# Performance work log

Measured on AMD Instinct MI355X. Metric: run time of the kernel, lower is better.

The kernel has to match this reference:

```python
import jax, jax.numpy as jnp
import numpy as np

N, E = 4096, 32768
NI, EI, D, EH = 64, 16, 64, 128
NUM_STEPS = 3


def setup_inputs() -> dict:
    key = jax.random.key(0)
    ks = jax.random.split(key, 24)

    def w(k, shape, fan_in):
        return (jax.random.normal(k, shape, jnp.float32) / np.float32(np.sqrt(fan_in)))

    return {
        "node_feats": jax.random.normal(ks[0], (N, NI), jnp.float32),
        "edge_attr": jax.random.normal(ks[1], (E, EI), jnp.float32),
        "edge_index": jax.random.randint(ks[2], (2, E), 0, N),
        # project_node_feats: Linear(NI -> D)
        "W_p": w(ks[3], (NI, D), NI), "b_p": jnp.zeros((D,), jnp.float32),
        # project_edge_feats: Linear(EI -> EH)
        "W_pe": w(ks[4], (EI, EH), EI), "b_pe": jnp.zeros((EH,), jnp.float32),
        # edge_network (NNConv nn): Linear(EH -> D*D)
        "W_nn": w(ks[5], (EH, D * D), EH), "b_nn": jnp.zeros((D * D,), jnp.float32),
        # NNConv root weight + bias
        "W_root": w(ks[6], (D, D), D), "b_conv": jnp.zeros((D,), jnp.float32),
        # GRU (single layer), gate order r, z, n as in torch
        "w_ih": w(ks[7], (D, 3 * D), D), "w_hh": w(ks[8], (D, 3 * D), D),
        "b_ih": jnp.zeros((3 * D,), jnp.float32), "b_hh": jnp.zeros((3 * D,), jnp.float32),
        # edge_update_network: Linear(EH+2D -> EH), Linear(EH -> EH)
        "W_eu1": w(ks[9], (EH + 2 * D, EH), EH + 2 * D), "b_eu1": jnp.zeros((EH,), jnp.float32),
        "W_eu2": w(ks[10], (EH, EH), EH), "b_eu2": jnp.zeros((EH,), jnp.float32),
    }


def reference(node_feats, edge_attr, edge_index, W_p, b_p, W_pe, b_pe,
              W_nn, b_nn, W_root, b_conv, w_ih, w_hh, b_ih, b_hh,
              W_eu1, b_eu1, W_eu2, b_eu2):
    relu = jax.nn.relu
    row, col = edge_index[0], edge_index[1]  # source, target
    n_nodes = node_feats.shape[0]
    d = W_root.shape[0]

    h = relu(node_feats @ W_p + b_p)          # (N, D) projected node feats
    hidden = h                                  # GRU hidden state
    e = relu(edge_attr @ W_pe + b_pe)          # (E, EH) projected edge feats

    for _ in range(NUM_STEPS):
        # NNConv: per-edge weight matrix from edge MLP (dropout=0 in eval)
        We = relu(e @ W_nn + b_nn).reshape(-1, d, d)      # (E, D, D)
        msg = jnp.einsum('ed,edf->ef', h[row], We)        # gather + per-edge matmul
        agg = jax.ops.segment_sum(msg, col, num_segments=n_nodes)  # scatter-add
        m = relu(agg + h @ W_root + b_conv)                # conv output + activation

        # GRU cell (torch gate order: r, z, n)
        gi = m @ w_ih + b_ih
        gh = hidden @ w_hh + b_hh
        ir, iz, i_n = jnp.split(gi, 3, axis=-1)
        hr, hz, h_n = jnp.split(gh, 3, axis=-1)
        r = jax.nn.sigmoid(ir + hr)
        z = jax.nn.sigmoid(iz + hz)
        ncand = jnp.tanh(i_n + r * h_n)
        hidden = (1.0 - z) * ncand + z * hidden
        h = hidden

        # edge update: cat(h[row], h[col], e) -> 2-layer MLP
        ei = jnp.concatenate([h[row], h[col], e], axis=1)
        e = relu(relu(ei @ W_eu1 + b_eu1) @ W_eu2 + b_eu2)

    return h, e
```

## Files before the change

### kernel.cpp

```cpp
#include <hip/hip_runtime.h>
#include <stdint.h>

typedef __attribute__((ext_vector_type(8))) _Float16 f16x8;
typedef __attribute__((ext_vector_type(4))) float f32x4;

#define N_NODES 4096
#define N_EDGES 32768

__device__ __forceinline__ float sigm(float x) { return 1.f / (1.f + __expf(-x)); }

__device__ __forceinline__ f16x8 packh8(const float* p) {
  f16x8 r;
#pragma unroll
  for (int i = 0; i < 8; ++i) r[i] = (_Float16)p[i];
  return r;
}

__global__ void prep_all(const float* __restrict__ Wnn,
                         const float* __restrict__ We1,
                         const float* __restrict__ We2,
                         _Float16* __restrict__ WnnT,
                         _Float16* __restrict__ We1T,
                         _Float16* __restrict__ We2T) {
  __shared__ float tile[128][33];
  const int b = blockIdx.x, t = threadIdx.x;
  if (b < 128) {
    const int nb = b * 32;
    for (int i = 0; i < 16; ++i) {
      int g = i * 256 + t;
      int k = g >> 5, j = g & 31;
      tile[k][j] = Wnn[(size_t)k * 4096 + nb + j];
    }
    __syncthreads();
    for (int i = 0; i < 16; ++i) {
      int g = i * 256 + t;
      int j = g >> 7, k = g & 127;
      WnnT[(size_t)(nb + j) * 128 + k] = (_Float16)tile[k][j];
    }
  } else {
    int idx = (b - 128) * 256 + t;
    if (idx < 32768) {
      int n = idx >> 8, k = idx & 255;
      We1T[idx] = (_Float16)We1[(size_t)k * 128 + n];
    } else {
      int j = idx - 32768;
      int n = j >> 7, k = j & 127;
      We2T[j] = (_Float16)We2[(size_t)k * 128 + n];
    }
  }
}

__global__ void csr_zero(int* __restrict__ rowcnt) {
  rowcnt[blockIdx.x * 256 + threadIdx.x] = 0;
}
__global__ void csr_count(const int* __restrict__ eidx, int* __restrict__ rowcnt) {
  int e = blockIdx.x * 256 + threadIdx.x;
  atomicAdd(&rowcnt[eidx[N_EDGES + e]], 1);
}
__global__ void csr_scan(const int* __restrict__ rowcnt,
                         int* __restrict__ rowptr, int* __restrict__ cursor) {
  __shared__ int part[1024];
  const int t = threadIdx.x;
  const int base = t * 4;
  int s0 = rowcnt[base], s1 = rowcnt[base + 1], s2 = rowcnt[base + 2], s3 = rowcnt[base + 3];
  int sum = s0 + s1 + s2 + s3;
  part[t] = sum;
  __syncthreads();
  for (int off = 1; off < 1024; off <<= 1) {
    int v = (t >= off) ? part[t - off] : 0;
    __syncthreads();
    part[t] += v;
    __syncthreads();
  }
  int excl = part[t] - sum;
  int p0 = excl, p1 = excl + s0, p2 = excl + s0 + s1, p3 = excl + s0 + s1 + s2;
  rowptr[base] = p0; rowptr[base + 1] = p1; rowptr[base + 2] = p2; rowptr[base + 3] = p3;
  cursor[base] = p0; cursor[base + 1] = p1; cursor[base + 2] = p2; cursor[base + 3] = p3;
  if (t == 0) rowptr[4096] = N_EDGES;
}
__global__ void csr_fill(const int* __restrict__ eidx, int* __restrict__ cursor,
                         int* __restrict__ eids) {
  int e = blockIdx.x * 256 + threadIdx.x;
  int slot = atomicAdd(&cursor[eidx[N_EDGES + e]], 1);
  eids[slot] = e;
}

__global__ void proj_node_f(const float* __restrict__ nf,
                            const float* __restrict__ Wp,
                            const float* __restrict__ bp,
                            float* __restrict__ h) {
  int idx = blockIdx.x * 256 + threadIdx.x;
  int n = idx >> 6, c = idx & 63;
  float acc = bp[c];
  for (int k = 0; k < 64; ++k)
    acc = fmaf(nf[n * 64 + k], Wp[k * 64 + c], acc);
  h[idx] = fmaxf(acc, 0.f);
}

__launch_bounds__(256)
__global__ void proj_edge_f2(const float* __restrict__ ea,
                             const float* __restrict__ Wpe,
                             const float* __restrict__ bpe,
                             float* __restrict__ e) {
  __shared__ float sw[16 * 128];
  __shared__ float sb[128];
  __shared__ float sa[32][17];
  const int t = threadIdx.x;
  const int ebase = blockIdx.x * 32;
  for (int g = t; g < 2048; g += 256) sw[g] = Wpe[g];
  if (t < 128) sb[t] = bpe[t];
  for (int g = t; g < 512; g += 256) {
    int r = g >> 4, k = g & 15;
    sa[r][k] = ea[(size_t)(ebase + r) * 16 + k];
  }
  __syncthreads();
  int c = t & 127, eg = t >> 7;
  float wc[16];
#pragma unroll
  for (int k = 0; k < 16; ++k) wc[k] = sw[k * 128 + c];
  float bv = sb[c];
#pragma unroll
  for (int i = 0; i < 16; ++i) {
    int ee = eg * 16 + i;
    float acc = bv;
#pragma unroll
    for (int k = 0; k < 16; ++k) acc = fmaf(sa[ee][k], wc[k], acc);
    e[(size_t)(ebase + ee) * 128 + c] = fmaxf(acc, 0.f);
  }
}

__launch_bounds__(512, 1)
__global__ void fused_msg_m(const float* __restrict__ ebf,
                            const float* __restrict__ hid,
                            const _Float16* __restrict__ WnnT,
                            const float* __restrict__ bnn,
                            const int* __restrict__ eidx,
                            _Float16* __restrict__ msgbuf) {
  __shared__ __align__(16) _Float16 Ae[128 * 128];
  __shared__ __align__(16) float Hs[64 * 132];
  const int t = threadIdx.x;
  const int w = t >> 6, l = t & 63, l15 = l & 15, q = l >> 4;
  const int fw = w & 3;
  const int eh = w >> 2;
  const int ebase = blockIdx.x * 128;
  const int rot = (blockIdx.x * 2 + w) & 15;

#pragma unroll
  for (int i = 0; i < 4; ++i) {
    int g = i * 512 + t;
    int e = g >> 4, d4 = g & 15;
    int r = eidx[ebase + e];
    float4 v = *(const float4*)&hid[(size_t)r * 64 + d4 * 4];
    Hs[(d4 * 4 + 0) * 132 + e] = v.x;
    Hs[(d4 * 4 + 1) * 132 + e] = v.y;
    Hs[(d4 * 4 + 2) * 132 + e] = v.z;
    Hs[(d4 * 4 + 3) * 132 + e] = v.w;
  }
#pragma unroll
  for (int i = 0; i < 4; ++i) {
    int g = i * 512 + t;
    int e = g >> 4, kg = g & 15;
    f16x8 v = packh8(&ebf[(size_t)(ebase + e) * 128 + kg * 8]);
    int kgp = kg ^ (e & 15);
    *(f16x8*)&Ae[e * 128 + kgp * 8] = v;
  }

  float msg[4][4];
#pragma unroll
  for (int m = 0; m < 4; ++m)
#pragma unroll
    for (int rr = 0; rr < 4; ++rr) msg[m][rr] = 0.f;

  __syncthreads();

  int aoff = 0;
  asm volatile("" : "+v"(aoff));

  const _Float16* wb = WnnT + (size_t)(fw * 16 + l15) * 128 + q * 8;

#pragma unroll 1
  for (int dgi = 0; dgi < 16; ++dgi) {
    const int dgr = (dgi + rot) & 15;
    f16x8 bb[4][4];
#pragma unroll
    for (int c = 0; c < 4; ++c) {
      const _Float16* p = wb + (size_t)(dgr * 4 + c) * 8192;
#pragma unroll
      for (int kk = 0; kk < 4; ++kk) bb[c][kk] = *(const f16x8*)(p + kk * 32);
    }
    float bnv[4];
#pragma unroll
    for (int c = 0; c < 4; ++c) bnv[c] = bnn[(dgr * 4 + c) * 64 + fw * 16 + l15];

#pragma unroll
    for (int m = 0; m < 4; ++m) {
      const int arow = (eh * 64 + m * 16 + l15) * 128 + aoff;
      f32x4 C[4];
#pragma unroll
      for (int c = 0; c < 4; ++c)
        C[c] = (f32x4){bnv[c], bnv[c], bnv[c], bnv[c]};
#pragma unroll
      for (int kk = 0; kk < 4; ++kk) {
        int kgp = (kk * 4 + q) ^ l15;
        f16x8 a = *(const f16x8*)&Ae[arow + kgp * 8];
#pragma unroll
        for (int c = 0; c < 4; ++c)
          C[c] = __builtin_amdgcn_mfma_f32_16x16x32_f16(a, bb[c][kk], C[c], 0, 0, 0);
      }
#pragma unroll
      for (int c = 0; c < 4; ++c) {
        int d = dgr * 4 + c;
        float4 hv = *(const float4*)&Hs[d * 132 + eh * 64 + m * 16 + q * 4];
        msg[m][0] = fmaf(hv.x, fmaxf(C[c][0], 0.f), msg[m][0]);
        msg[m][1] = fmaf(hv.y, fmaxf(C[c][1], 0.f), msg[m][1]);
        msg[m][2] = fmaf(hv.z, fmaxf(C[c][2], 0.f), msg[m][2]);
        msg[m][3] = fmaf(hv.w, fmaxf(C[c][3], 0.f), msg[m][3]);
      }
    }
  }

#pragma unroll
  for (int m = 0; m < 4; ++m)
#pragma unroll
    for (int rr = 0; rr < 4; ++rr) {
      int e = ebase + eh * 64 + m * 16 + q * 4 + rr;
      msgbuf[(size_t)e * 64 + fw * 16 + l15] = (_Float16)msg[m][rr];
    }
}

__launch_bounds__(256)
__global__ void node_update_g(const _Float16* __restrict__ msgbuf,
                              const int* __restrict__ rowptr,
                              const int* __restrict__ eids,
                              float* __restrict__ hid,
                              const float* __restrict__ Wroot,
                              const float* __restrict__ bconv,
                              const float* __restrict__ wih,
                              const float* __restrict__ whh,
                              const float* __restrict__ bih,
                              const float* __restrict__ bhh) {
  __shared__ __align__(16) float shT[64 * 20];
  __shared__ __align__(16) float smT[64 * 20];
  __shared__ __align__(16) float sg[16 * 384];
  __shared__ __align__(16) float sW[64 * 64];
  const int t = threadIdx.x;
  const int nb = blockIdx.x * 16;

#pragma unroll
  for (int i = 0; i < 4; ++i) {
    int g = i * 256 + t;
    *(float4*)&sW[g * 4] = *(const float4*)&Wroot[g * 4];
  }
#pragma unroll
  for (int i = 0; i < 4; ++i) {
    int idx = i * 256 + t;
    int nl = idx >> 6, dc = idx & 63;
    shT[dc * 20 + nl] = hid[(size_t)(nb + nl) * 64 + dc];
  }
  __syncthreads();

#pragma unroll
  for (int i = 0; i < 4; ++i) {
    int idx = i * 256 + t;
    int nl = idx >> 6, dc = idx & 63;
    int n = nb + nl;
    float acc = bconv[dc];
    int r0 = rowptr[n], r1 = rowptr[n + 1];
    for (int j = r0; j < r1; ++j)
      acc += (float)msgbuf[(size_t)eids[j] * 64 + dc];
    for (int k = 0; k < 64; ++k)
      acc = fmaf(shT[k * 20 + nl], sW[k * 64 + dc], acc);
    smT[dc * 20 + nl] = fmaxf(acc, 0.f);
  }
  __syncthreads();

  for (int p = 0; p < 2; ++p) {
    int j2 = p * 256 + t;
    if (j2 < 384) {
      bool is_ih = (j2 < 192);
      int col = is_ih ? j2 : j2 - 192;
      const float* W = is_ih ? wih : whh;
      float bias = is_ih ? bih[col] : bhh[col];
      const float* inT = is_ih ? smT : shT;
      float a[16];
#pragma unroll
      for (int nl = 0; nl < 16; ++nl) a[nl] = bias;
      for (int k = 0; k < 64; ++k) {
        float wv = W[k * 192 + col];
        float4 v0 = *(const float4*)&inT[k * 20 + 0];
        float4 v1 = *(const float4*)&inT[k * 20 + 4];
        float4 v2 = *(const float4*)&inT[k * 20 + 8];
        float4 v3 = *(const float4*)&inT[k * 20 + 12];
        a[0]  = fmaf(v0.x, wv, a[0]);  a[1]  = fmaf(v0.y, wv, a[1]);
        a[2]  = fmaf(v0.z, wv, a[2]);  a[3]  = fmaf(v0.w, wv, a[3]);
        a[4]  = fmaf(v1.x, wv, a[4]);  a[5]  = fmaf(v1.y, wv, a[5]);
        a[6]  = fmaf(v1.z, wv, a[6]);  a[7]  = fmaf(v1.w, wv, a[7]);
        a[8]  = fmaf(v2.x, wv, a[8]);  a[9]  = fmaf(v2.y, wv, a[9]);
        a[10] = fmaf(v2.z, wv, a[10]); a[11] = fmaf(v2.w, wv, a[11]);
        a[12] = fmaf(v3.x, wv, a[12]); a[13] = fmaf(v3.y, wv, a[13]);
        a[14] = fmaf(v3.z, wv, a[14]); a[15] = fmaf(v3.w, wv, a[15]);
      }
#pragma unroll
      for (int nl = 0; nl < 16; ++nl) sg[nl * 384 + j2] = a[nl];
    }
  }
  __syncthreads();

#pragma unroll
  for (int i = 0; i < 4; ++i) {
    int idx = i * 256 + t;
    int nl = idx >> 6, dc = idx & 63;
    const float* g = &sg[nl * 384];
    float ir = g[dc], iz = g[64 + dc], in_ = g[128 + dc];
    float hr = g[192 + dc], hz = g[256 + dc], hn = g[320 + dc];
    float r = sigm(ir + hr), z = sigm(iz + hz);
    float nc = tanhf(in_ + r * hn);
    hid[(size_t)nb * 64 + idx] = (1.f - z) * nc + z * shT[dc * 20 + nl];
  }
}

__launch_bounds__(256)
__global__ void edge_mlp_m(const float* __restrict__ hid,
                           float* __restrict__ ebf,
                           const int* __restrict__ eidx,
                           const _Float16* __restrict__ We1T,
                           const float* __restrict__ be1,
                           const _Float16* __restrict__ We2T,
                           const float* __restrict__ be2) {
  __shared__ _Float16 As[64 * 264];
  __shared__ _Float16 Ts[64 * 136];
  const int t = threadIdx.x;
  const int w = t >> 6, l = t & 63, l15 = l & 15, q = l >> 4;
  const int mbase = blockIdx.x * 64;

  for (int g = t; g < 2048; g += 256) {
    int r = g >> 5, kg = g & 31;
    int e = mbase + r;
    const float* src;
    if (kg < 8)       src = &hid[(size_t)eidx[e] * 64 + kg * 8];
    else if (kg < 16) src = &hid[(size_t)eidx[N_EDGES + e] * 64 + (kg - 8) * 8];
    else              src = &ebf[(size_t)e * 128 + (kg - 16) * 8];
    *(f16x8*)&As[r * 264 + kg * 8] = packh8(src);
  }
  __syncthreads();

  f32x4 zero4 = {0.f, 0.f, 0.f, 0.f};
  f32x4 acc[4][2];
#pragma unroll
  for (int m = 0; m < 4; ++m)
#pragma unroll
    for (int nn = 0; nn < 2; ++nn) acc[m][nn] = zero4;

#pragma unroll
  for (int kc = 0; kc < 4; ++kc)
#pragma unroll
    for (int kk = 0; kk < 2; ++kk) {
      int ko = kc * 64 + kk * 32 + q * 8;
      f16x8 b0 = *(const f16x8*)(We1T + (size_t)(w * 32 + l15) * 256 + ko);
      f16x8 b1 = *(const f16x8*)(We1T + (size_t)(w * 32 + 16 + l15) * 256 + ko);
#pragma unroll
      for (int m = 0; m < 4; ++m) {
        f16x8 a = *(const f16x8*)&As[(m * 16 + l15) * 264 + ko];
        acc[m][0] = __builtin_amdgcn_mfma_f32_16x16x32_f16(a, b0, acc[m][0], 0, 0, 0);
        acc[m][1] = __builtin_amdgcn_mfma_f32_16x16x32_f16(a, b1, acc[m][1], 0, 0, 0);
      }
    }

#pragma unroll
  for (int m = 0; m < 4; ++m)
#pragma unroll
    for (int nn = 0; nn < 2; ++nn) {
      int col = w * 32 + nn * 16 + l15;
      float bv = be1[col];
#pragma unroll
      for (int rr = 0; rr < 4; ++rr) {
        int row = m * 16 + q * 4 + rr;
        Ts[row * 136 + col] = (_Float16)fmaxf(acc[m][nn][rr] + bv, 0.f);
      }
    }
  __syncthreads();

  f32x4 acc2[4][2];
#pragma unroll
  for (int m = 0; m < 4; ++m)
#pragma unroll
    for (int nn = 0; nn < 2; ++nn) acc2[m][nn] = zero4;

#pragma unroll
  for (int kc = 0; kc < 2; ++kc)
#pragma unroll
    for (int kk = 0; kk < 2; ++kk) {
      int ko = kc * 64 + kk * 32 + q * 8;
      f16x8 b0 = *(const f16x8*)(We2T + (size_t)(w * 32 + l15) * 128 + ko);
      f16x8 b1 = *(const f16x8*)(We2T + (size_t)(w * 32 + 16 + l15) * 128 + ko);
#pragma unroll
      for (int m = 0; m < 4; ++m) {
        f16x8 a = *(const f16x8*)&Ts[(m * 16 + l15) * 136 + ko];
        acc2[m][0] = __builtin_amdgcn_mfma_f32_16x16x32_f16(a, b0, acc2[m][0], 0, 0, 0);
        acc2[m][1] = __builtin_amdgcn_mfma_f32_16x16x32_f16(a, b1, acc2[m][1], 0, 0, 0);
      }
    }

#pragma unroll
  for (int m = 0; m < 4; ++m)
#pragma unroll
    for (int nn = 0; nn < 2; ++nn) {
      int col = w * 32 + nn * 16 + l15;
      float bv = be2[col];
#pragma unroll
      for (int rr = 0; rr < 4; ++rr) {
        int row = mbase + m * 16 + q * 4 + rr;
        ebf[(size_t)row * 128 + col] = fmaxf(acc2[m][nn][rr] + bv, 0.f);
      }
    }
}

extern "C" void kernel_launch(void* const* d_in, const int* in_sizes, int n_in,
                              void* d_out, int out_size, void* d_ws, size_t ws_size,
                              hipStream_t stream) {
  const float* nf    = (const float*)d_in[0];
  const float* ea    = (const float*)d_in[1];
  const int*   eidx  = (const int*)d_in[2];
  const float* Wp    = (const float*)d_in[3];
  const float* bp    = (const float*)d_in[4];
  const float* Wpe   = (const float*)d_in[5];
  const float* bpe   = (const float*)d_in[6];
  const float* Wnn   = (const float*)d_in[7];
  const float* bnn   = (const float*)d_in[8];
  const float* Wroot = (const float*)d_in[9];
  const float* bconv = (const float*)d_in[10];
  const float* wih   = (const float*)d_in[11];
  const float* whh   = (const float*)d_in[12];
  const float* bih   = (const float*)d_in[13];
  const float* bhh   = (const float*)d_in[14];
  const float* We1   = (const float*)d_in[15];
  const float* be1   = (const float*)d_in[16];
  const float* We2   = (const float*)d_in[17];
  const float* be2   = (const float*)d_in[18];

  float* hid = (float*)d_out;
  float* ebf = (float*)d_out + 4096 * 64;

  char* ws = (char*)d_ws;
  _Float16* WnnT   = (_Float16*)(ws + 0);
  _Float16* We1T   = (_Float16*)(ws + 1048576);
  _Float16* We2T   = (_Float16*)(ws + 1114112);
  _Float16* msgbuf = (_Float16*)(ws + 1146880);
  int*      rowptr = (int*)(ws + 5341184);
  int*      cursor = (int*)(ws + 5357696);
  int*      eids   = (int*)(ws + 5374080);

  prep_all<<<320, 256, 0, stream>>>(Wnn, We1, We2, WnnT, We1T, We2T);
  proj_node_f<<<1024, 256, 0, stream>>>(nf, Wp, bp, hid);
  proj_edge_f2<<<1024, 256, 0, stream>>>(ea, Wpe, bpe, ebf);

  csr_zero<<<16, 256, 0, stream>>>(cursor);
  csr_count<<<128, 256, 0, stream>>>(eidx, cursor);
  csr_scan<<<1, 1024, 0, stream>>>(cursor, rowptr, cursor);
  csr_fill<<<128, 256, 0, stream>>>(eidx, cursor, eids);

  for (int s = 0; s < 3; ++s) {
    fused_msg_m<<<256, 512, 0, stream>>>(ebf, hid, WnnT, bnn, eidx, msgbuf);
    node_update_g<<<256, 256, 0, stream>>>(msgbuf, rowptr, eids, hid, Wroot, bconv,
                                           wih, whh, bih, bhh);
    edge_mlp_m<<<512, 256, 0, stream>>>(hid, ebf, eidx, We1T, be1, We2T, be2);
  }
}
```

Measured before the change: 468.7 us.

## Merge setup kernels and preload edge-MLP weights into registers

Folds the CSR zeroing into the node-projection launch and the CSR counting into the edge-projection launch, cutting two kernel launches from the setup phase. The edge MLP kernel now loads all its We1/We2 B-fragments and biases into registers before the gather, so those global loads are issued early instead of inside the MFMA loops. The register preload raises per-thread register pressure, which the added launch bound of one block per SM is meant to accommodate, though that may limit occupancy.

```diff
diff --git a/kernel.cpp b/kernel.cpp
--- a/kernel.cpp
+++ b/kernel.cpp
@@ -50,13 +50,63 @@
   }
 }
 
-__global__ void csr_zero(int* __restrict__ rowcnt) {
-  rowcnt[blockIdx.x * 256 + threadIdx.x] = 0;
-}
-__global__ void csr_count(const int* __restrict__ eidx, int* __restrict__ rowcnt) {
-  int e = blockIdx.x * 256 + threadIdx.x;
-  atomicAdd(&rowcnt[eidx[N_EDGES + e]], 1);
-}
+__global__ void zero_projnode(const float* __restrict__ nf,
+                              const float* __restrict__ Wp,
+                              const float* __restrict__ bp,
+                              float* __restrict__ h,
+                              int* __restrict__ rowcnt) {
+  const int b = blockIdx.x, t = threadIdx.x;
+  if (b < 16) {
+    rowcnt[b * 256 + t] = 0;
+    return;
+  }
+  int idx = (b - 16) * 256 + t;
+  int n = idx >> 6, c = idx & 63;
+  float acc = bp[c];
+  for (int k = 0; k < 64; ++k)
+    acc = fmaf(nf[n * 64 + k], Wp[k * 64 + c], acc);
+  h[idx] = fmaxf(acc, 0.f);
+}
+
+__launch_bounds__(256)
+__global__ void count_projedge(const float* __restrict__ ea,
+                               const float* __restrict__ Wpe,
+                               const float* __restrict__ bpe,
+                               float* __restrict__ e,
+                               const int* __restrict__ eidx,
+                               int* __restrict__ rowcnt) {
+  __shared__ float sw[16 * 128];
+  __shared__ float sb[128];
+  __shared__ float sa[32][17];
+  const int b = blockIdx.x, t = threadIdx.x;
+  if (b < 128) {
+    int ed = b * 256 + t;
+    atomicAdd(&rowcnt[eidx[N_EDGES + ed]], 1);
+    return;
+  }
+  const int ebase = (b - 128) * 32;
+  for (int g = t; g < 2048; g += 256) sw[g] = Wpe[g];
+  if (t < 128) sb[t] = bpe[t];
+  for (int g = t; g < 512; g += 256) {
+    int r = g >> 4, k = g & 15;
+    sa[r][k] = ea[(size_t)(ebase + r) * 16 + k];
+  }
+  __syncthreads();
+  int c = t & 127, eg = t >> 7;
+  float wc[16];
+#pragma unroll
+  for (int k = 0; k < 16; ++k) wc[k] = sw[k * 128 + c];
+  float bv = sb[c];
+#pragma unroll
+  for (int i = 0; i < 16; ++i) {
+    int ee = eg * 16 + i;
+    float acc = bv;
+#pragma unroll
+    for (int k = 0; k < 16; ++k) acc = fmaf(sa[ee][k], wc[k], acc);
+    e[(size_t)(ebase + ee) * 128 + c] = fmaxf(acc, 0.f);
+  }
+}
+
 __global__ void csr_scan(const int* __restrict__ rowcnt,
                          int* __restrict__ rowptr, int* __restrict__ cursor) {
   __shared__ int part[1024];
@@ -83,50 +133,6 @@
   int e = blockIdx.x * 256 + threadIdx.x;
   int slot = atomicAdd(&cursor[eidx[N_EDGES + e]], 1);
   eids[slot] = e;
-}
-
-__global__ void proj_node_f(const float* __restrict__ nf,
-                            const float* __restrict__ Wp,
-                            const float* __restrict__ bp,
-                            float* __restrict__ h) {
-  int idx = blockIdx.x * 256 + threadIdx.x;
-  int n = idx >> 6, c = idx & 63;
-  float acc = bp[c];
-  for (int k = 0; k < 64; ++k)
-    acc = fmaf(nf[n * 64 + k], Wp[k * 64 + c], acc);
-  h[idx] = fmaxf(acc, 0.f);
-}
-
-__launch_bounds__(256)
-__global__ void proj_edge_f2(const float* __restrict__ ea,
-                             const float* __restrict__ Wpe,
-                             const float* __restrict__ bpe,
-                             float* __restrict__ e) {
-  __shared__ float sw[16 * 128];
-  __shared__ float sb[128];
-  __shared__ float sa[32][17];
-  const int t = threadIdx.x;
-  const int ebase = blockIdx.x * 32;
-  for (int g = t; g < 2048; g += 256) sw[g] = Wpe[g];
-  if (t < 128) sb[t] = bpe[t];
-  for (int g = t; g < 512; g += 256) {
-    int r = g >> 4, k = g & 15;
-    sa[r][k] = ea[(size_t)(ebase + r) * 16 + k];
-  }
-  __syncthreads();
-  int c = t & 127, eg = t >> 7;
-  float wc[16];
-#pragma unroll
-  for (int k = 0; k < 16; ++k) wc[k] = sw[k * 128 + c];
-  float bv = sb[c];
-#pragma unroll
-  for (int i = 0; i < 16; ++i) {
-    int ee = eg * 16 + i;
-    float acc = bv;
-#pragma unroll
-    for (int k = 0; k < 16; ++k) acc = fmaf(sa[ee][k], wc[k], acc);
-    e[(size_t)(ebase + ee) * 128 + c] = fmaxf(acc, 0.f);
-  }
 }
 
 __launch_bounds__(512, 1)
@@ -319,7 +325,7 @@
   }
 }
 
-__launch_bounds__(256)
+__launch_bounds__(256, 1)
 __global__ void edge_mlp_m(const float* __restrict__ hid,
                            float* __restrict__ ebf,
                            const int* __restrict__ eidx,
@@ -333,6 +339,27 @@
   const int w = t >> 6, l = t & 63, l15 = l & 15, q = l >> 4;
   const int mbase = blockIdx.x * 64;
 
+  f16x8 B1[4][2][2];
+#pragma unroll
+  for (int kc = 0; kc < 4; ++kc)
+#pragma unroll
+    for (int kk = 0; kk < 2; ++kk) {
+      int ko = kc * 64 + kk * 32 + q * 8;
+      B1[kc][kk][0] = *(const f16x8*)(We1T + (size_t)(w * 32 + l15) * 256 + ko);
+      B1[kc][kk][1] = *(const f16x8*)(We1T + (size_t)(w * 32 + 16 + l15) * 256 + ko);
+    }
+  f16x8 B2[2][2][2];
+#pragma unroll
+  for (int kc = 0; kc < 2; ++kc)
+#pragma unroll
+    for (int kk = 0; kk < 2; ++kk) {
+      int ko = kc * 64 + kk * 32 + q * 8;
+      B2[kc][kk][0] = *(const f16x8*)(We2T + (size_t)(w * 32 + l15) * 128 + ko);
+      B2[kc][kk][1] = *(const f16x8*)(We2T + (size_t)(w * 32 + 16 + l15) * 128 + ko);
+    }
+  float bv1_0 = be1[w * 32 + l15],      bv1_1 = be1[w * 32 + 16 + l15];
+  float bv2_0 = be2[w * 32 + l15],      bv2_1 = be2[w * 32 + 16 + l15];
+
   for (int g = t; g < 2048; g += 256) {
     int r = g >> 5, kg = g & 31;
     int e = mbase + r;
@@ -356,13 +383,11 @@
 #pragma unroll
     for (int kk = 0; kk < 2; ++kk) {
       int ko = kc * 64 + kk * 32 + q * 8;
-      f16x8 b0 = *(const f16x8*)(We1T + (size_t)(w * 32 + l15) * 256 + ko);
-      f16x8 b1 = *(const f16x8*)(We1T + (size_t)(w * 32 + 16 + l15) * 256 + ko);
 #pragma unroll
       for (int m = 0; m < 4; ++m) {
         f16x8 a = *(const f16x8*)&As[(m * 16 + l15) * 264 + ko];
-        acc[m][0] = __builtin_amdgcn_mfma_f32_16x16x32_f16(a, b0, acc[m][0], 0, 0, 0);
-        acc[m][1] = __builtin_amdgcn_mfma_f32_16x16x32_f16(a, b1, acc[m][1], 0, 0, 0);
+        acc[m][0] = __builtin_amdgcn_mfma_f32_16x16x32_f16(a, B1[kc][kk][0], acc[m][0], 0, 0, 0);
+        acc[m][1] = __builtin_amdgcn_mfma_f32_16x16x32_f16(a, B1[kc][kk][1], acc[m][1], 0, 0, 0);
       }
     }
 
@@ -371,7 +396,7 @@
 #pragma unroll
     for (int nn = 0; nn < 2; ++nn) {
       int col = w * 32 + nn * 16 + l15;
-      float bv = be1[col];
+      float bv = nn ? bv1_1 : bv1_0;
 #pragma unroll
       for (int rr = 0; rr < 4; ++rr) {
         int row = m * 16 + q * 4 + rr;
@@ -391,13 +416,11 @@
 #pragma unroll
     for (int kk = 0; kk < 2; ++kk) {
       int ko = kc * 64 + kk * 32 + q * 8;
-      f16x8 b0 = *(const f16x8*)(We2T + (size_t)(w * 32 + l15) * 128 + ko);
-      f16x8 b1 = *(const f16x8*)(We2T + (size_t)(w * 32 + 16 + l15) * 128 + ko);
 #pragma unroll
       for (int m = 0; m < 4; ++m) {
         f16x8 a = *(const f16x8*)&Ts[(m * 16 + l15) * 136 + ko];
-        acc2[m][0] = __builtin_amdgcn_mfma_f32_16x16x32_f16(a, b0, acc2[m][0], 0, 0, 0);
-        acc2[m][1] = __builtin_amdgcn_mfma_f32_16x16x32_f16(a, b1, acc2[m][1], 0, 0, 0);
+        acc2[m][0] = __builtin_amdgcn_mfma_f32_16x16x32_f16(a, B2[kc][kk][0], acc2[m][0], 0, 0, 0);
+        acc2[m][1] = __builtin_amdgcn_mfma_f32_16x16x32_f16(a, B2[kc][kk][1], acc2[m][1], 0, 0, 0);
       }
     }
 
@@ -406,7 +429,7 @@
 #pragma unroll
     for (int nn = 0; nn < 2; ++nn) {
       int col = w * 32 + nn * 16 + l15;
-      float bv = be2[col];
+      float bv = nn ? bv2_1 : bv2_0;
 #pragma unroll
       for (int rr = 0; rr < 4; ++rr) {
         int row = mbase + m * 16 + q * 4 + rr;
@@ -451,11 +474,8 @@
   int*      eids   = (int*)(ws + 5374080);
 
   prep_all<<<320, 256, 0, stream>>>(Wnn, We1, We2, WnnT, We1T, We2T);
-  proj_node_f<<<1024, 256, 0, stream>>>(nf, Wp, bp, hid);
-  proj_edge_f2<<<1024, 256, 0, stream>>>(ea, Wpe, bpe, ebf);
-
-  csr_zero<<<16, 256, 0, stream>>>(cursor);
-  csr_count<<<128, 256, 0, stream>>>(eidx, cursor);
+  zero_projnode<<<1040, 256, 0, stream>>>(nf, Wp, bp, hid, cursor);
+  count_projedge<<<1152, 256, 0, stream>>>(ea, Wpe, bpe, ebf, eidx, cursor);
   csr_scan<<<1, 1024, 0, stream>>>(cursor, rowptr, cursor);
   csr_fill<<<128, 256, 0, stream>>>(eidx, cursor, eids);
 
```

New measurement: 472.5 us. No clear change (+0.8%).
